# Optimization experiments

Hardware: AMD Instinct MI355X
Metric: run time of the kernel (lower is better)

## Reference

```python
import jax, jax.numpy as jnp
import numpy as np

B, T, D, H = 2, 2048, 2048, 16
HD = D // H  # 128
HALF = HD // 2  # 64


def _apply_rotary(x, cos, sin):
    """x: (B,H,T,HD); cos/sin: (T, HD//2). Interleaved rotation matching torch ref."""
    half = x.shape[-1] // 2
    x1, x2 = x[..., :half], x[..., half:]
    c = cos[None, None, :, :]
    s = sin[None, None, :, :]
    # stack on last axis then flatten -> out[...,2i]=x1*c-x2*s, out[...,2i+1]=x1*s+x2*c
    return jnp.stack([x1 * c - x2 * s, x1 * s + x2 * c], axis=-1).reshape(x.shape)


def setup_inputs() -> dict:
    key = jax.random.key(0)
    k1, k2, k3 = jax.random.split(key, 3)
    x = jax.random.normal(k1, (B, T, D), dtype=jnp.float32)
    # realistic RoPE tables: theta = 10000^{-2i/HD}
    inv_freq = 1.0 / (10000.0 ** (np.arange(0, HALF, dtype=np.float32) * 2.0 / HD))
    ang = np.arange(T, dtype=np.float32)[:, None] * inv_freq[None, :]  # (T, HALF)
    cos = jnp.asarray(np.cos(ang), dtype=jnp.float32)
    sin = jnp.asarray(np.sin(ang), dtype=jnp.float32)
    Wqkv = jax.random.normal(k2, (D, 3 * D), dtype=jnp.float32) * (D ** -0.5)
    Wproj = jax.random.normal(k3, (D, D), dtype=jnp.float32) * (D ** -0.5)
    return {"x": x, "cos": cos, "sin": sin, "Wqkv": Wqkv, "Wproj": Wproj}


def reference(x, cos, sin, Wqkv, Wproj):
    b, t, d = x.shape
    qkv = (x @ Wqkv).reshape(b, t, 3, H, HD)
    q = jnp.transpose(qkv[:, :, 0], (0, 2, 1, 3))  # (B,H,T,HD)
    k = jnp.transpose(qkv[:, :, 1], (0, 2, 1, 3))
    v = jnp.transpose(qkv[:, :, 2], (0, 2, 1, 3))
    q = _apply_rotary(q, cos, sin)
    k = _apply_rotary(k, cos, sin)
    scale = 1.0 / jnp.sqrt(jnp.asarray(HD, dtype=x.dtype))
    scores = jnp.einsum("bhqd,bhkd->bhqk", q, k) * scale
    causal = jnp.tril(jnp.ones((t, t), dtype=bool))
    scores = jnp.where(causal[None, None], scores, jnp.finfo(x.dtype).min)
    attn = jax.nn.softmax(scores, axis=-1)
    out = jnp.einsum("bhqk,bhkd->bhqd", attn, v)
    out = jnp.transpose(out, (0, 2, 1, 3)).reshape(b, t, d)
    return out @ Wproj
```

## Files before the change

kernel.cpp:

```cpp
#include <hip/hip_runtime.h>
#include <hip/hip_bf16.h>

#define B_  2
#define T_  2048
#define D_  2048
#define H_  16
#define HD_ 128
#define NT_ 4096
#define D3_ 6144

typedef __bf16 bf16;
typedef bf16 bf16x2 __attribute__((ext_vector_type(2)));
typedef bf16 bf16x4 __attribute__((ext_vector_type(4)));
typedef bf16 bf16x8 __attribute__((ext_vector_type(8)));
typedef float floatx4 __attribute__((ext_vector_type(4)));

__device__ __forceinline__ void gl_lds16(const bf16* g, bf16* l) {
    __builtin_amdgcn_global_load_lds((const __attribute__((address_space(1))) void*)g,
                                     (__attribute__((address_space(3))) void*)l, 16, 0, 0);
}

__global__ __launch_bounds__(256) void k_cvt(const float* __restrict__ in, bf16* __restrict__ out, int n4) {
    int i = blockIdx.x * 256 + threadIdx.x;
    if (i >= n4) return;
    float4 v = ((const float4*)in)[i];
    bf16x4 o = { (bf16)v.x, (bf16)v.y, (bf16)v.z, (bf16)v.w };
    ((bf16x4*)out)[i] = o;
}

__global__ __launch_bounds__(256) void k_tcvt(const float* __restrict__ in, bf16* __restrict__ out, int R, int C) {
    __shared__ float tile[64][65];
    int c0 = blockIdx.x * 64, r0 = blockIdx.y * 64;
    int tid = threadIdx.x;
#pragma unroll
    for (int i = 0; i < 16; i++) {
        int idx = tid + i * 256, r = idx >> 6, c = idx & 63;
        tile[r][c] = in[(size_t)(r0 + r) * C + (c0 + c)];
    }
    __syncthreads();
#pragma unroll
    for (int i = 0; i < 16; i++) {
        int idx = tid + i * 256, r = idx >> 6, c = idx & 63;
        out[(size_t)(c0 + r) * R + (r0 + c)] = (bf16)tile[c][r];
    }
}

template <typename OutT>
__global__ __launch_bounds__(256) void k_gemm_bt(const bf16* __restrict__ A, const bf16* __restrict__ Bt,
                                                 OutT* __restrict__ C, int M, int N, int K) {
    __shared__ bf16 As[128 * 32];
    __shared__ bf16 Bs[128 * 32];
    const int tid = threadIdx.x, w = tid >> 6, lane = tid & 63;
    const int quad = lane >> 4, l16 = lane & 15;
    const int n0 = blockIdx.x * 128, m0 = blockIdx.y * 128;
    const int wr = (w >> 1) * 64, wc = (w & 1) * 64;
    const bf16* Ab = A + (size_t)m0 * K;
    const bf16* Bb = Bt + (size_t)n0 * K;
    const int srow = lane >> 2, scol = (lane & 3) * 8;
    floatx4 acc[4][4] = {};
    for (int k0 = 0; k0 < K; k0 += 32) {
        __syncthreads();
#pragma unroll
        for (int i = 0; i < 2; i++) {
            int ch = w * 2 + i;
            gl_lds16(Ab + (size_t)(ch * 16 + srow) * K + k0 + scol, As + ch * 512);
            gl_lds16(Bb + (size_t)(ch * 16 + srow) * K + k0 + scol, Bs + ch * 512);
        }
        __syncthreads();
        bf16x8 af[4], bfr[4];
#pragma unroll
        for (int mt = 0; mt < 4; mt++) af[mt] = *(const bf16x8*)(As + (wr + mt * 16 + l16) * 32 + quad * 8);
#pragma unroll
        for (int nt = 0; nt < 4; nt++) bfr[nt] = *(const bf16x8*)(Bs + (wc + nt * 16 + l16) * 32 + quad * 8);
#pragma unroll
        for (int mt = 0; mt < 4; mt++)
#pragma unroll
            for (int nt = 0; nt < 4; nt++)
                acc[mt][nt] = __builtin_amdgcn_mfma_f32_16x16x32_bf16(af[mt], bfr[nt], acc[mt][nt], 0, 0, 0);
    }
#pragma unroll
    for (int mt = 0; mt < 4; mt++)
#pragma unroll
        for (int nt = 0; nt < 4; nt++)
#pragma unroll
            for (int r = 0; r < 4; r++) {
                int row = m0 + wr + mt * 16 + quad * 4 + r;
                int col = n0 + wc + nt * 16 + l16;
                C[(size_t)row * N + col] = (OutT)acc[mt][nt][r];
            }
}

__global__ __launch_bounds__(256) void k_rope_scatter(const bf16* __restrict__ qkv,
                                                      const float* __restrict__ cosp, const float* __restrict__ sinp,
                                                      bf16* __restrict__ Qg, bf16* __restrict__ Kg, bf16* __restrict__ VTg) {
    __shared__ bf16 vt[128][66];
    int blk = blockIdx.x;
    int tb = blk & 31, h = (blk >> 5) & 15, b = blk >> 9;
    int t0 = tb * 64;
    int tid = threadIdx.x;
    int i = tid & 63, rr = tid >> 6;
#pragma unroll
    for (int it = 0; it < 16; it++) {
        int r = it * 4 + rr;
        int t = t0 + r;
        float c = cosp[t * 64 + i], s = sinp[t * 64 + i];
        size_t qbase = (size_t)(b * T_ + t) * D3_ + h * HD_;
        size_t obase = ((size_t)(b * H_ + h) * T_ + t) * HD_ + 2 * i;
        float x1 = (float)qkv[qbase + i], x2 = (float)qkv[qbase + 64 + i];
        bf16x2 qo = { (bf16)(x1 * c - x2 * s), (bf16)(x1 * s + x2 * c) };
        *(bf16x2*)(Qg + obase) = qo;
        x1 = (float)qkv[qbase + D_ + i]; x2 = (float)qkv[qbase + D_ + 64 + i];
        bf16x2 ko = { (bf16)(x1 * c - x2 * s), (bf16)(x1 * s + x2 * c) };
        *(bf16x2*)(Kg + obase) = ko;
    }
#pragma unroll
    for (int it = 0; it < 32; it++) {
        int idx = it * 256 + tid;
        int r = idx >> 7, d = idx & 127;
        vt[d][r] = qkv[(size_t)(b * T_ + t0 + r) * D3_ + 2 * D_ + h * HD_ + d];
    }
    __syncthreads();
#pragma unroll
    for (int it = 0; it < 32; it++) {
        int idx = it * 256 + tid;
        int d = idx >> 6, tt = idx & 63;
        VTg[((size_t)(b * H_ + h) * HD_ + d) * T_ + t0 + tt] = vt[d][tt];
    }
}

__global__ __launch_bounds__(256, 2) void k_flash(const bf16* __restrict__ Qg, const bf16* __restrict__ Kg,
                                                  const bf16* __restrict__ VTg, bf16* __restrict__ Og) {
    __shared__ bf16 Ksh[64 * 128];
    __shared__ bf16 Vsh[128 * 64];
    __shared__ bf16 Psh[4 * 32 * 72];
    const int b1 = blockIdx.x;
    const int bh = b1 & 31;
    const int qt = (b1 < 256) ? (15 - (b1 >> 5)) : ((b1 - 256) >> 5);
    const int tid = threadIdx.x, w = tid >> 6, lane = tid & 63;
    const int quad = lane >> 4, l16 = lane & 15;
    const float scale2 = 0.08838834764831845f * 1.4426950408889634f;
    const int wrow = w * 32;
    const bf16* Qb = Qg + ((size_t)bh * T_ + qt * 128) * HD_;
    bf16x8 qf[2][4];
#pragma unroll
    for (int mt = 0; mt < 2; mt++)
#pragma unroll
        for (int kc = 0; kc < 4; kc++)
            qf[mt][kc] = *(const bf16x8*)(Qb + (size_t)(wrow + mt * 16 + l16) * HD_ + kc * 32 + quad * 8);
    floatx4 oacc[2][8] = {};
    floatx4 lacc[2] = {};
    bf16* Pw = Psh + w * 32 * 72;
    const int nkt = 2 * (qt + 1);
    for (int kt = 0; kt < nkt; kt++) {
        __syncthreads();
        const bf16* Kt = Kg + ((size_t)bh * T_ + kt * 64) * HD_;
        const bf16* Vt = VTg + (size_t)bh * HD_ * T_ + kt * 64;
#pragma unroll
        for (int i = 0; i < 4; i++) {
            int ch = w * 4 + i;
            {
                int row = ch * 4 + (lane >> 4);
                int c = (lane & 15) ^ (row & 7);
                gl_lds16(Kt + (size_t)row * HD_ + c * 8, Ksh + ch * 512);
            }
            {
                int row = ch * 8 + (lane >> 3);
                int c = (lane & 7) ^ (row & 7);
                gl_lds16(Vt + (size_t)row * T_ + c * 8, Vsh + ch * 512);
            }
        }
        __syncthreads();
        floatx4 s[2][4] = {};
#pragma unroll
        for (int kc = 0; kc < 4; kc++) {
            bf16x8 kf[4];
#pragma unroll
            for (int nt = 0; nt < 4; nt++)
                kf[nt] = *(const bf16x8*)(Ksh + (nt * 16 + l16) * 128 + (((kc * 4 + quad) ^ (l16 & 7)) * 8));
#pragma unroll
            for (int mt = 0; mt < 2; mt++)
#pragma unroll
                for (int nt = 0; nt < 4; nt++)
                    s[mt][nt] = __builtin_amdgcn_mfma_f32_16x16x32_bf16(qf[mt][kc], kf[nt], s[mt][nt], 0, 0, 0);
        }
        const bool diag = (kt >= 2 * qt);
#pragma unroll
        for (int mt = 0; mt < 2; mt++)
#pragma unroll
            for (int nt = 0; nt < 4; nt++)
#pragma unroll
                for (int r = 0; r < 4; r++) {
                    float v = s[mt][nt][r] * scale2;
                    if (diag) {
                        int gr = qt * 128 + wrow + mt * 16 + quad * 4 + r;
                        int gc = kt * 64 + nt * 16 + l16;
                        if (gc > gr) v = -1e30f;
                    }
                    float p = exp2f(v);
                    s[mt][nt][r] = p;
                    lacc[mt][r] += p;
                }
#pragma unroll
        for (int mt = 0; mt < 2; mt++)
#pragma unroll
            for (int nt = 0; nt < 4; nt++)
#pragma unroll
                for (int r = 0; r < 4; r++)
                    Pw[(mt * 16 + quad * 4 + r) * 72 + nt * 16 + l16] = (bf16)s[mt][nt][r];
#pragma unroll
        for (int kc2 = 0; kc2 < 2; kc2++) {
            bf16x8 pf[2];
#pragma unroll
            for (int mt = 0; mt < 2; mt++)
                pf[mt] = *(const bf16x8*)(Pw + (mt * 16 + l16) * 72 + kc2 * 32 + quad * 8);
#pragma unroll
            for (int nt2 = 0; nt2 < 8; nt2++) {
                bf16x8 vf = *(const bf16x8*)(Vsh + (nt2 * 16 + l16) * 64 + (((kc2 * 4 + quad) ^ (l16 & 7)) * 8));
#pragma unroll
                for (int mt = 0; mt < 2; mt++)
                    oacc[mt][nt2] = __builtin_amdgcn_mfma_f32_16x16x32_bf16(pf[mt], vf, oacc[mt][nt2], 0, 0, 0);
            }
        }
    }
    const int b = bh >> 4, h = bh & 15;
#pragma unroll
    for (int mt = 0; mt < 2; mt++) {
        float inv[4];
#pragma unroll
        for (int r = 0; r < 4; r++) {
            float l = lacc[mt][r];
            l += __shfl_xor(l, 1); l += __shfl_xor(l, 2);
            l += __shfl_xor(l, 4); l += __shfl_xor(l, 8);
            inv[r] = 1.0f / l;
        }
#pragma unroll
        for (int nt2 = 0; nt2 < 8; nt2++)
#pragma unroll
            for (int r = 0; r < 4; r++) {
                int t = qt * 128 + wrow + mt * 16 + quad * 4 + r;
                int c = h * HD_ + nt2 * 16 + l16;
                Og[(size_t)(b * T_ + t) * D_ + c] = (bf16)(oacc[mt][nt2][r] * inv[r]);
            }
    }
}

extern "C" void kernel_launch(void* const* d_in, const int* in_sizes, int n_in,
                              void* d_out, int out_size, void* d_ws, size_t ws_size,
                              hipStream_t stream) {
    const float* x     = (const float*)d_in[0];
    const float* cosp  = (const float*)d_in[1];
    const float* sinp  = (const float*)d_in[2];
    const float* Wqkv  = (const float*)d_in[3];
    const float* Wproj = (const float*)d_in[4];
    float* out = (float*)d_out;
    char* ws = (char*)d_ws;
    bf16* xb     = (bf16*)(ws);
    bf16* WqkvT  = (bf16*)(ws + (size_t)(16u  << 20));
    bf16* WprojT = (bf16*)(ws + (size_t)(40u  << 20));
    bf16* qkv    = (bf16*)(ws + (size_t)(48u  << 20));
    bf16* Qg     = (bf16*)(ws + (size_t)(96u  << 20));
    bf16* Kg     = (bf16*)(ws + (size_t)(112u << 20));
    bf16* VTg    = (bf16*)(ws + (size_t)(128u << 20));
    bf16* Og     = xb;

    k_cvt<<<dim3(NT_ * D_ / 4 / 256), 256, 0, stream>>>(x, xb, NT_ * D_ / 4);
    k_tcvt<<<dim3(D3_ / 64, D_ / 64), 256, 0, stream>>>(Wqkv, WqkvT, D_, D3_);
    k_tcvt<<<dim3(D_ / 64, D_ / 64), 256, 0, stream>>>(Wproj, WprojT, D_, D_);
    k_gemm_bt<bf16><<<dim3(D3_ / 128, NT_ / 128), 256, 0, stream>>>(xb, WqkvT, qkv, NT_, D3_, D_);
    k_rope_scatter<<<dim3(B_ * H_ * T_ / 64), 256, 0, stream>>>(qkv, cosp, sinp, Qg, Kg, VTg);
    k_flash<<<dim3(512), 256, 0, stream>>>(Qg, Kg, VTg, Og);
    k_gemm_bt<float><<<dim3(D_ / 128, NT_ / 128), 256, 0, stream>>>(Og, WprojT, out, NT_, D_, D_);
}
```

Baseline: 428.3 us.

## Fuse prep kernels, fold RoPE into QKV GEMM, keep P in registers in flash

Merges the x conversion and both weight transpose-conversions into one launch. Moves RoPE and the V transpose into the epilogue of the QKV GEMM through an LDS staging tile, which removes the intermediate qkv buffer round trip and one launch. The attention kernel now computes S transposed so the probabilities can feed the PV MFMA straight from registers as fp16 (16x16x16 f16). That drops the P shared-memory round trip and uses fp16 for V and P, at the cost of a larger LDS footprint in the GEMM and different rounding.

```diff
diff --git a/kernel.cpp b/kernel.cpp
--- a/kernel.cpp
+++ b/kernel.cpp
@@ -10,28 +10,38 @@
 #define D3_ 6144
 
 typedef __bf16 bf16;
+typedef _Float16 f16;
 typedef bf16 bf16x2 __attribute__((ext_vector_type(2)));
 typedef bf16 bf16x4 __attribute__((ext_vector_type(4)));
 typedef bf16 bf16x8 __attribute__((ext_vector_type(8)));
+typedef f16  f16x2  __attribute__((ext_vector_type(2)));
+typedef f16  f16x4  __attribute__((ext_vector_type(4)));
 typedef float floatx4 __attribute__((ext_vector_type(4)));
 
-__device__ __forceinline__ void gl_lds16(const bf16* g, bf16* l) {
+__device__ __forceinline__ void gl_lds16(const void* g, void* l) {
     __builtin_amdgcn_global_load_lds((const __attribute__((address_space(1))) void*)g,
                                      (__attribute__((address_space(3))) void*)l, 16, 0, 0);
 }
 
-__global__ __launch_bounds__(256) void k_cvt(const float* __restrict__ in, bf16* __restrict__ out, int n4) {
-    int i = blockIdx.x * 256 + threadIdx.x;
-    if (i >= n4) return;
-    float4 v = ((const float4*)in)[i];
-    bf16x4 o = { (bf16)v.x, (bf16)v.y, (bf16)v.z, (bf16)v.w };
-    ((bf16x4*)out)[i] = o;
-}
-
-__global__ __launch_bounds__(256) void k_tcvt(const float* __restrict__ in, bf16* __restrict__ out, int R, int C) {
+__global__ __launch_bounds__(256) void k_prep(const float* __restrict__ x,
+                                              const float* __restrict__ Wqkv, const float* __restrict__ Wproj,
+                                              bf16* __restrict__ xb, bf16* __restrict__ WqkvT, bf16* __restrict__ WprojT) {
+    int blk = blockIdx.x;
+    int tid = threadIdx.x;
+    if (blk < 8192) {
+        int i = blk * 256 + tid;
+        float4 v = ((const float4*)x)[i];
+        bf16x4 o = { (bf16)v.x, (bf16)v.y, (bf16)v.z, (bf16)v.w };
+        ((bf16x4*)xb)[i] = o;
+        return;
+    }
     __shared__ float tile[64][65];
-    int c0 = blockIdx.x * 64, r0 = blockIdx.y * 64;
-    int tid = threadIdx.x;
+    const float* in; bf16* out; int C, bx;
+    if (blk < 8192 + 3072) { bx = blk - 8192; in = Wqkv; out = WqkvT; C = D3_; }
+    else                   { bx = blk - 8192 - 3072; in = Wproj; out = WprojT; C = D_; }
+    const int R = D_;
+    int nbx = C / 64;
+    int c0 = (bx % nbx) * 64, r0 = (bx / nbx) * 64;
 #pragma unroll
     for (int i = 0; i < 16; i++) {
         int idx = tid + i * 256, r = idx >> 6, c = idx & 63;
@@ -42,6 +52,72 @@
     for (int i = 0; i < 16; i++) {
         int idx = tid + i * 256, r = idx >> 6, c = idx & 63;
         out[(size_t)(c0 + r) * R + (r0 + c)] = (bf16)tile[c][r];
+    }
+}
+
+__global__ __launch_bounds__(256) void k_gemm_qkv(const bf16* __restrict__ A, const bf16* __restrict__ Bt,
+                                                  const float* __restrict__ cosp, const float* __restrict__ sinp,
+                                                  bf16* __restrict__ Qg, bf16* __restrict__ Kg, f16* __restrict__ VTg) {
+    __shared__ bf16 As[128 * 32];
+    __shared__ bf16 Bs[128 * 32];
+    __shared__ bf16 stage[128 * 130];
+    const int tid = threadIdx.x, w = tid >> 6, lane = tid & 63;
+    const int quad = lane >> 4, l16 = lane & 15;
+    const int n0 = blockIdx.x * 128, m0 = blockIdx.y * 128;
+    const int wr = (w >> 1) * 64, wc = (w & 1) * 64;
+    const bf16* Ab = A + (size_t)m0 * D_;
+    const bf16* Bb = Bt + (size_t)n0 * D_;
+    const int srow = lane >> 2, scol = (lane & 3) * 8;
+    floatx4 acc[4][4] = {};
+    for (int k0 = 0; k0 < D_; k0 += 32) {
+        __syncthreads();
+#pragma unroll
+        for (int i = 0; i < 2; i++) {
+            int ch = w * 2 + i;
+            gl_lds16(Ab + (size_t)(ch * 16 + srow) * D_ + k0 + scol, As + ch * 512);
+            gl_lds16(Bb + (size_t)(ch * 16 + srow) * D_ + k0 + scol, Bs + ch * 512);
+        }
+        __syncthreads();
+        bf16x8 af[4], bfr[4];
+#pragma unroll
+        for (int mt = 0; mt < 4; mt++) af[mt] = *(const bf16x8*)(As + (wr + mt * 16 + l16) * 32 + quad * 8);
+#pragma unroll
+        for (int nt = 0; nt < 4; nt++) bfr[nt] = *(const bf16x8*)(Bs + (wc + nt * 16 + l16) * 32 + quad * 8);
+#pragma unroll
+        for (int mt = 0; mt < 4; mt++)
+#pragma unroll
+            for (int nt = 0; nt < 4; nt++)
+                acc[mt][nt] = __builtin_amdgcn_mfma_f32_16x16x32_bf16(af[mt], bfr[nt], acc[mt][nt], 0, 0, 0);
+    }
+    __syncthreads();
+#pragma unroll
+    for (int mt = 0; mt < 4; mt++)
+#pragma unroll
+        for (int nt = 0; nt < 4; nt++)
+#pragma unroll
+            for (int r = 0; r < 4; r++)
+                stage[(wr + mt * 16 + quad * 4 + r) * 130 + wc + nt * 16 + l16] = (bf16)acc[mt][nt][r];
+    __syncthreads();
+    const int type = n0 >> 11, h = (n0 & 2047) >> 7;
+    const int b = m0 >> 11, t0 = m0 & 2047;
+    if (type < 2) {
+        bf16* out = (type == 0 ? Qg : Kg) + ((size_t)(b * H_ + h) * T_ + t0) * HD_;
+#pragma unroll
+        for (int it = 0; it < 32; it++) {
+            int idx = it * 256 + tid, tl = idx >> 6, i = idx & 63;
+            float c = cosp[(t0 + tl) * 64 + i], s = sinp[(t0 + tl) * 64 + i];
+            float x1 = (float)stage[tl * 130 + i], x2 = (float)stage[tl * 130 + 64 + i];
+            bf16x2 o = { (bf16)(x1 * c - x2 * s), (bf16)(x1 * s + x2 * c) };
+            *(bf16x2*)(out + (size_t)tl * HD_ + 2 * i) = o;
+        }
+    } else {
+        f16* out = VTg + (size_t)(b * H_ + h) * HD_ * T_ + t0;
+#pragma unroll
+        for (int it = 0; it < 32; it++) {
+            int idx = it * 256 + tid, d = idx >> 6, tp = (idx & 63) * 2;
+            f16x2 o = { (f16)(float)stage[tp * 130 + d], (f16)(float)stage[(tp + 1) * 130 + d] };
+            *(f16x2*)(out + (size_t)d * T_ + tp) = o;
+        }
     }
 }
 
@@ -90,49 +166,10 @@
             }
 }
 
-__global__ __launch_bounds__(256) void k_rope_scatter(const bf16* __restrict__ qkv,
-                                                      const float* __restrict__ cosp, const float* __restrict__ sinp,
-                                                      bf16* __restrict__ Qg, bf16* __restrict__ Kg, bf16* __restrict__ VTg) {
-    __shared__ bf16 vt[128][66];
-    int blk = blockIdx.x;
-    int tb = blk & 31, h = (blk >> 5) & 15, b = blk >> 9;
-    int t0 = tb * 64;
-    int tid = threadIdx.x;
-    int i = tid & 63, rr = tid >> 6;
-#pragma unroll
-    for (int it = 0; it < 16; it++) {
-        int r = it * 4 + rr;
-        int t = t0 + r;
-        float c = cosp[t * 64 + i], s = sinp[t * 64 + i];
-        size_t qbase = (size_t)(b * T_ + t) * D3_ + h * HD_;
-        size_t obase = ((size_t)(b * H_ + h) * T_ + t) * HD_ + 2 * i;
-        float x1 = (float)qkv[qbase + i], x2 = (float)qkv[qbase + 64 + i];
-        bf16x2 qo = { (bf16)(x1 * c - x2 * s), (bf16)(x1 * s + x2 * c) };
-        *(bf16x2*)(Qg + obase) = qo;
-        x1 = (float)qkv[qbase + D_ + i]; x2 = (float)qkv[qbase + D_ + 64 + i];
-        bf16x2 ko = { (bf16)(x1 * c - x2 * s), (bf16)(x1 * s + x2 * c) };
-        *(bf16x2*)(Kg + obase) = ko;
-    }
-#pragma unroll
-    for (int it = 0; it < 32; it++) {
-        int idx = it * 256 + tid;
-        int r = idx >> 7, d = idx & 127;
-        vt[d][r] = qkv[(size_t)(b * T_ + t0 + r) * D3_ + 2 * D_ + h * HD_ + d];
-    }
-    __syncthreads();
-#pragma unroll
-    for (int it = 0; it < 32; it++) {
-        int idx = it * 256 + tid;
-        int d = idx >> 6, tt = idx & 63;
-        VTg[((size_t)(b * H_ + h) * HD_ + d) * T_ + t0 + tt] = vt[d][tt];
-    }
-}
-
 __global__ __launch_bounds__(256, 2) void k_flash(const bf16* __restrict__ Qg, const bf16* __restrict__ Kg,
-                                                  const bf16* __restrict__ VTg, bf16* __restrict__ Og) {
+                                                  const f16* __restrict__ VTg, bf16* __restrict__ Og) {
     __shared__ bf16 Ksh[64 * 128];
-    __shared__ bf16 Vsh[128 * 64];
-    __shared__ bf16 Psh[4 * 32 * 72];
+    __shared__ f16  Vsh[128 * 64];
     const int b1 = blockIdx.x;
     const int bh = b1 & 31;
     const int qt = (b1 < 256) ? (15 - (b1 >> 5)) : ((b1 - 256) >> 5);
@@ -147,14 +184,13 @@
 #pragma unroll
         for (int kc = 0; kc < 4; kc++)
             qf[mt][kc] = *(const bf16x8*)(Qb + (size_t)(wrow + mt * 16 + l16) * HD_ + kc * 32 + quad * 8);
-    floatx4 oacc[2][8] = {};
-    floatx4 lacc[2] = {};
-    bf16* Pw = Psh + w * 32 * 72;
+    floatx4 oaccT[8][2] = {};
+    float lsum[2] = { 0.f, 0.f };
     const int nkt = 2 * (qt + 1);
     for (int kt = 0; kt < nkt; kt++) {
         __syncthreads();
         const bf16* Kt = Kg + ((size_t)bh * T_ + kt * 64) * HD_;
-        const bf16* Vt = VTg + (size_t)bh * HD_ * T_ + kt * 64;
+        const f16*  Vt = VTg + (size_t)bh * HD_ * T_ + kt * 64;
 #pragma unroll
         for (int i = 0; i < 4; i++) {
             int ch = w * 4 + i;
@@ -170,77 +206,61 @@
             }
         }
         __syncthreads();
-        floatx4 s[2][4] = {};
-#pragma unroll
-        for (int kc = 0; kc < 4; kc++) {
-            bf16x8 kf[4];
-#pragma unroll
-            for (int nt = 0; nt < 4; nt++)
-                kf[nt] = *(const bf16x8*)(Ksh + (nt * 16 + l16) * 128 + (((kc * 4 + quad) ^ (l16 & 7)) * 8));
-#pragma unroll
-            for (int mt = 0; mt < 2; mt++)
-#pragma unroll
-                for (int nt = 0; nt < 4; nt++)
-                    s[mt][nt] = __builtin_amdgcn_mfma_f32_16x16x32_bf16(qf[mt][kc], kf[nt], s[mt][nt], 0, 0, 0);
-        }
         const bool diag = (kt >= 2 * qt);
-#pragma unroll
-        for (int mt = 0; mt < 2; mt++)
-#pragma unroll
-            for (int nt = 0; nt < 4; nt++)
-#pragma unroll
-                for (int r = 0; r < 4; r++) {
-                    float v = s[mt][nt][r] * scale2;
-                    if (diag) {
-                        int gr = qt * 128 + wrow + mt * 16 + quad * 4 + r;
-                        int gc = kt * 64 + nt * 16 + l16;
-                        if (gc > gr) v = -1e30f;
-                    }
-                    float p = exp2f(v);
-                    s[mt][nt][r] = p;
-                    lacc[mt][r] += p;
+        f16x4 pf[2][4];
+#pragma unroll
+        for (int nt = 0; nt < 4; nt++) {
+            floatx4 s0 = {}, s1 = {};
+#pragma unroll
+            for (int kc = 0; kc < 4; kc++) {
+                bf16x8 kf = *(const bf16x8*)(Ksh + (nt * 16 + l16) * 128 + (((kc * 4 + quad) ^ (l16 & 7)) * 8));
+                s0 = __builtin_amdgcn_mfma_f32_16x16x32_bf16(kf, qf[0][kc], s0, 0, 0, 0);
+                s1 = __builtin_amdgcn_mfma_f32_16x16x32_bf16(kf, qf[1][kc], s1, 0, 0, 0);
+            }
+#pragma unroll
+            for (int r = 0; r < 4; r++) {
+                float v0 = s0[r] * scale2, v1 = s1[r] * scale2;
+                if (diag) {
+                    int gk = kt * 64 + nt * 16 + quad * 4 + r;
+                    if (gk > qt * 128 + wrow + l16) v0 = -1e30f;
+                    if (gk > qt * 128 + wrow + 16 + l16) v1 = -1e30f;
                 }
-#pragma unroll
-        for (int mt = 0; mt < 2; mt++)
-#pragma unroll
-            for (int nt = 0; nt < 4; nt++)
-#pragma unroll
-                for (int r = 0; r < 4; r++)
-                    Pw[(mt * 16 + quad * 4 + r) * 72 + nt * 16 + l16] = (bf16)s[mt][nt][r];
-#pragma unroll
-        for (int kc2 = 0; kc2 < 2; kc2++) {
-            bf16x8 pf[2];
-#pragma unroll
-            for (int mt = 0; mt < 2; mt++)
-                pf[mt] = *(const bf16x8*)(Pw + (mt * 16 + l16) * 72 + kc2 * 32 + quad * 8);
-#pragma unroll
-            for (int nt2 = 0; nt2 < 8; nt2++) {
-                bf16x8 vf = *(const bf16x8*)(Vsh + (nt2 * 16 + l16) * 64 + (((kc2 * 4 + quad) ^ (l16 & 7)) * 8));
+                float p0 = exp2f(v0), p1 = exp2f(v1);
+                lsum[0] += p0; lsum[1] += p1;
+                pf[0][nt][r] = (f16)p0; pf[1][nt][r] = (f16)p1;
+            }
+        }
+#pragma unroll
+        for (int nt = 0; nt < 4; nt++)
+#pragma unroll
+            for (int dt = 0; dt < 8; dt++) {
+                int row = dt * 16 + l16;
+                f16x4 vf = *(const f16x4*)(Vsh + row * 64 + (((nt * 2 + (quad >> 1)) ^ (row & 7)) * 8) + (quad & 1) * 4);
 #pragma unroll
                 for (int mt = 0; mt < 2; mt++)
-                    oacc[mt][nt2] = __builtin_amdgcn_mfma_f32_16x16x32_bf16(pf[mt], vf, oacc[mt][nt2], 0, 0, 0);
-            }
-        }
+                    oaccT[dt][mt] = __builtin_amdgcn_mfma_f32_16x16x16f16(vf, pf[mt][nt], oaccT[dt][mt], 0, 0, 0);
+            }
     }
     const int b = bh >> 4, h = bh & 15;
+    float inv[2];
 #pragma unroll
     for (int mt = 0; mt < 2; mt++) {
-        float inv[4];
-#pragma unroll
-        for (int r = 0; r < 4; r++) {
-            float l = lacc[mt][r];
-            l += __shfl_xor(l, 1); l += __shfl_xor(l, 2);
-            l += __shfl_xor(l, 4); l += __shfl_xor(l, 8);
-            inv[r] = 1.0f / l;
-        }
-#pragma unroll
-        for (int nt2 = 0; nt2 < 8; nt2++)
-#pragma unroll
-            for (int r = 0; r < 4; r++) {
-                int t = qt * 128 + wrow + mt * 16 + quad * 4 + r;
-                int c = h * HD_ + nt2 * 16 + l16;
-                Og[(size_t)(b * T_ + t) * D_ + c] = (bf16)(oacc[mt][nt2][r] * inv[r]);
-            }
+        float l = lsum[mt];
+        l += __shfl_xor(l, 16);
+        l += __shfl_xor(l, 32);
+        inv[mt] = 1.0f / l;
+    }
+#pragma unroll
+    for (int mt = 0; mt < 2; mt++) {
+        int t = qt * 128 + wrow + mt * 16 + l16;
+#pragma unroll
+        for (int dt = 0; dt < 8; dt++) {
+            bf16x4 o;
+#pragma unroll
+            for (int r = 0; r < 4; r++) o[r] = (bf16)(oaccT[dt][mt][r] * inv[mt]);
+            int c = h * HD_ + dt * 16 + quad * 4;
+            *(bf16x4*)(Og + (size_t)(b * T_ + t) * D_ + c) = o;
+        }
     }
 }
 
@@ -255,19 +275,15 @@
     float* out = (float*)d_out;
     char* ws = (char*)d_ws;
     bf16* xb     = (bf16*)(ws);
-    bf16* WqkvT  = (bf16*)(ws + (size_t)(16u  << 20));
-    bf16* WprojT = (bf16*)(ws + (size_t)(40u  << 20));
-    bf16* qkv    = (bf16*)(ws + (size_t)(48u  << 20));
-    bf16* Qg     = (bf16*)(ws + (size_t)(96u  << 20));
-    bf16* Kg     = (bf16*)(ws + (size_t)(112u << 20));
-    bf16* VTg    = (bf16*)(ws + (size_t)(128u << 20));
+    bf16* WqkvT  = (bf16*)(ws + (size_t)(16u << 20));
+    bf16* WprojT = (bf16*)(ws + (size_t)(40u << 20));
+    bf16* Qg     = (bf16*)(ws + (size_t)(48u << 20));
+    bf16* Kg     = (bf16*)(ws + (size_t)(64u << 20));
+    f16*  VTg    = (f16*) (ws + (size_t)(80u << 20));
     bf16* Og     = xb;
 
-    k_cvt<<<dim3(NT_ * D_ / 4 / 256), 256, 0, stream>>>(x, xb, NT_ * D_ / 4);
-    k_tcvt<<<dim3(D3_ / 64, D_ / 64), 256, 0, stream>>>(Wqkv, WqkvT, D_, D3_);
-    k_tcvt<<<dim3(D_ / 64, D_ / 64), 256, 0, stream>>>(Wproj, WprojT, D_, D_);
-    k_gemm_bt<bf16><<<dim3(D3_ / 128, NT_ / 128), 256, 0, stream>>>(xb, WqkvT, qkv, NT_, D3_, D_);
-    k_rope_scatter<<<dim3(B_ * H_ * T_ / 64), 256, 0, stream>>>(qkv, cosp, sinp, Qg, Kg, VTg);
+    k_prep<<<dim3(8192 + 3072 + 1024), 256, 0, stream>>>(x, Wqkv, Wproj, xb, WqkvT, WprojT);
+    k_gemm_qkv<<<dim3(D3_ / 128, NT_ / 128), 256, 0, stream>>>(xb, WqkvT, cosp, sinp, Qg, Kg, VTg);
     k_flash<<<dim3(512), 256, 0, stream>>>(Qg, Kg, VTg, Og);
     k_gemm_bt<float><<<dim3(D_ / 128, NT_ / 128), 256, 0, stream>>>(Og, WprojT, out, NT_, D_, D_);
 }
```

Result: faster. 387.6 us (-9.5%).
